# Performance work log

Hardware: AMD Instinct MI355X
Metric: run time of the kernel (lower is better)

Reference implementation:

```python
import jax, jax.numpy as jnp
import numpy as np

NUM_ITERS = 10  # forward() runs power_iteration with num_iters=10


def setup_inputs() -> dict:
    key = jax.random.key(0)
    k1, k2 = jax.random.split(key)
    out_ch, in_ch, h, w = 2048, 2048, 3, 3
    conv_filter = jax.random.normal(k1, (out_ch, in_ch, h, w), dtype=jnp.float32) * 0.02
    u = jax.random.normal(k2, (1, in_ch * w), dtype=jnp.float32)
    u = u / jnp.linalg.norm(u, axis=1, keepdims=True)
    return {"conv_filter": conv_filter, "u": u}


def reference(conv_filter, u):
    out_ch, in_ch, h, w = conv_filter.shape
    # permute (0,2,1,3) then view as [out_ch*h, in_ch*w]
    W = jnp.transpose(conv_filter, (0, 2, 1, 3)).reshape(out_ch * h, in_ch * w)
    Ws = jax.lax.stop_gradient(W)  # power iteration vectors are detached

    def body(i, carry):
        u_n, _ = carry
        v = u_n @ Ws.T                                   # [1, out_ch*h]
        v_n = v / jnp.linalg.norm(v, axis=1, keepdims=True)
        u2 = v_n @ Ws                                    # [1, in_ch*w]
        u_n2 = u2 / jnp.linalg.norm(u2, axis=1, keepdims=True)
        return (u_n2, v_n)

    v0 = jnp.zeros((1, out_ch * h), dtype=conv_filter.dtype)  # overwritten in first iter
    u_n, v_n = jax.lax.fori_loop(0, NUM_ITERS, body, (u, v0))

    # sigma = v W u^T with u, v treated as constants (custom autograd Function)
    sigma = (v_n @ W) @ u_n.T                            # [1, 1]
    return jnp.sqrt(jnp.asarray(h * w, dtype=conv_filter.dtype)) * sigma
```

## Files before the change

kernel.cpp:

```cpp
#include <hip/hip_runtime.h>
#include <hip/hip_bf16.h>
#include <hip/hip_fp16.h>

#define OC_N     2048
#define IC_N     2048
#define RC       6144
#define OCSTRIDE 18432
#define UNSCALE  0.0000152587890625f

typedef float v2f __attribute__((ext_vector_type(2)));

__device__ __forceinline__ float wave_reduce(float x) {
#pragma unroll
    for (int off = 32; off > 0; off >>= 1) x += __shfl_down(x, off, 64);
    return x;
}

__global__ __launch_bounds__(256) void convert_q_kernel(
    const float* __restrict__ conv, unsigned char* __restrict__ Wq)
{
    const int t  = blockIdx.x * 256 + threadIdx.x;
    const int o8 = t * 8;
    const int r  = o8 / RC;
    const int c0 = o8 % RC;
    const int oc = r / 3, hh = r % 3;
    const float* base = conv + (size_t)oc * OCSTRIDE + hh * 3;
    float f[8];
#pragma unroll
    for (int e = 0; e < 8; ++e) {
        const int c  = c0 + e;
        const int ic = c / 3, ww = c - 3 * ic;
        f[e] = base[ic * 9 + ww] * 256.0f;
    }
    int lo = __builtin_amdgcn_cvt_pk_fp8_f32(f[0], f[1], 0, false);
    lo     = __builtin_amdgcn_cvt_pk_fp8_f32(f[2], f[3], lo, true);
    int hi = __builtin_amdgcn_cvt_pk_fp8_f32(f[4], f[5], 0, false);
    hi     = __builtin_amdgcn_cvt_pk_fp8_f32(f[6], f[7], hi, true);
    *reinterpret_cast<uint2*>(Wq + o8) = make_uint2((unsigned)lo, (unsigned)hi);
}

__global__ __launch_bounds__(256) void transpose_q_kernel(
    const unsigned char* __restrict__ Wq, unsigned char* __restrict__ WqT)
{
    __shared__ unsigned char tile[64][68];
    const int tid = threadIdx.x;
    const int tr  = blockIdx.x;
    const int tc  = blockIdx.y;

    const int r  = tid >> 2;
    const int cq = (tid & 3) * 16;
    const uint4 w = *reinterpret_cast<const uint4*>(
        Wq + (size_t)(tr * 64 + r) * RC + tc * 64 + cq);
    *reinterpret_cast<unsigned int*>(&tile[r][cq +  0]) = w.x;
    *reinterpret_cast<unsigned int*>(&tile[r][cq +  4]) = w.y;
    *reinterpret_cast<unsigned int*>(&tile[r][cq +  8]) = w.z;
    *reinterpret_cast<unsigned int*>(&tile[r][cq + 12]) = w.w;
    __syncthreads();

    const int orow = tid >> 2;
    const int ocq  = (tid & 3) * 16;
    unsigned int u32s[4];
#pragma unroll
    for (int wi = 0; wi < 4; ++wi) {
        const int ro = ocq + 4 * wi;
        u32s[wi] =  (unsigned int)tile[ro + 0][orow]
                 | ((unsigned int)tile[ro + 1][orow] << 8)
                 | ((unsigned int)tile[ro + 2][orow] << 16)
                 | ((unsigned int)tile[ro + 3][orow] << 24);
    }
    uint4 o = make_uint4(u32s[0], u32s[1], u32s[2], u32s[3]);
    *reinterpret_cast<uint4*>(WqT + (size_t)(tc * 64 + orow) * RC + tr * 64 + ocq) = o;
}

__device__ __forceinline__ float dot16(uint4 w, float4 a, float4 b, float4 c, float4 d) {
    float acc = 0.f;
    v2f f;
    f = __builtin_amdgcn_cvt_pk_f32_fp8(w.x, false); acc += f.x * a.x + f.y * a.y;
    f = __builtin_amdgcn_cvt_pk_f32_fp8(w.x, true);  acc += f.x * a.z + f.y * a.w;
    f = __builtin_amdgcn_cvt_pk_f32_fp8(w.y, false); acc += f.x * b.x + f.y * b.y;
    f = __builtin_amdgcn_cvt_pk_f32_fp8(w.y, true);  acc += f.x * b.z + f.y * b.w;
    f = __builtin_amdgcn_cvt_pk_f32_fp8(w.z, false); acc += f.x * c.x + f.y * c.y;
    f = __builtin_amdgcn_cvt_pk_f32_fp8(w.z, true);  acc += f.x * c.z + f.y * c.w;
    f = __builtin_amdgcn_cvt_pk_f32_fp8(w.w, false); acc += f.x * d.x + f.y * d.y;
    f = __builtin_amdgcn_cvt_pk_f32_fp8(w.w, true);  acc += f.x * d.z + f.y * d.w;
    return acc;
}

__device__ __forceinline__ void stage_x(const float* __restrict__ x,
                                        float4* __restrict__ x4, int tid) {
    const float4* s4 = reinterpret_cast<const float4*>(x);
#pragma unroll
    for (int k = 0; k < 6; ++k) {
        const int g = tid + 256 * k;
        x4[g + (g >> 2)] = s4[g];
    }
}

__device__ __forceinline__ void matvec_rows2(
    const unsigned char* __restrict__ W, const float4* __restrict__ x4,
    int rbase, int lane, float* out0, float* out1)
{
    const unsigned char* w0 = W + (size_t)rbase * RC;
    float acc0 = 0.f, acc1 = 0.f;
#pragma unroll
    for (int i = 0; i < 6; ++i) {
        const int slot = i * 320 + lane * 5;
        const float4 a = x4[slot + 0];
        const float4 b = x4[slot + 1];
        const float4 c = x4[slot + 2];
        const float4 d = x4[slot + 3];
        const uint4 wA = *reinterpret_cast<const uint4*>(w0 +      i * 1024 + lane * 16);
        const uint4 wB = *reinterpret_cast<const uint4*>(w0 + RC + i * 1024 + lane * 16);
        acc0 += dot16(wA, a, b, c, d);
        acc1 += dot16(wB, a, b, c, d);
    }
    *out0 = wave_reduce(acc0);
    *out1 = wave_reduce(acc1);
}

__global__ __launch_bounds__(256) void matvec_q_kernel(
    const unsigned char* __restrict__ W, const float* __restrict__ x,
    float* __restrict__ y, float scale)
{
    __shared__ float x_lds[7680];
    float4* x4 = reinterpret_cast<float4*>(x_lds);

    const int tid  = threadIdx.x;
    const int lane = tid & 63;
    const int wid  = tid >> 6;

    stage_x(x, x4, tid);
    __syncthreads();

    const int rbase = blockIdx.x * 8 + wid * 2;
    float a0, a1;
    matvec_rows2(W, x4, rbase, lane, &a0, &a1);
    if (lane == 0) { y[rbase] = a0 * scale; y[rbase + 1] = a1 * scale; }
}

__global__ __launch_bounds__(256) void final_kernel(
    const float* __restrict__ v, const float* __restrict__ t,
    const float* __restrict__ u, float* __restrict__ out)
{
    __shared__ float ssv[4];
    __shared__ float ssu[4];
    __shared__ float sdot[4];
    const int tid  = threadIdx.x;
    const int lane = tid & 63;
    const int wid  = tid >> 6;
    float sqv = 0.f, squ = 0.f, dot = 0.f;
#pragma unroll
    for (int k = 0; k < 24; ++k) {
        const float xv = v[tid + 256 * k];
        const float xt = t[tid + 256 * k];
        const float xu = u[tid + 256 * k];
        sqv += xv * xv;
        squ += xu * xu;
        dot += xv * xt;
    }
    sqv = wave_reduce(sqv);
    squ = wave_reduce(squ);
    dot = wave_reduce(dot);
    if (lane == 0) { ssv[wid] = sqv; ssu[wid] = squ; sdot[wid] = dot; }
    __syncthreads();
    if (tid == 0) {
        const float vs = ssv[0] + ssv[1] + ssv[2] + ssv[3];
        const float us = ssu[0] + ssu[1] + ssu[2] + ssu[3];
        const float dt = sdot[0] + sdot[1] + sdot[2] + sdot[3];
        out[0] = (3.0f / 256.0f) * dt * rsqrtf(vs) * rsqrtf(us);
    }
}

extern "C" void kernel_launch(void* const* d_in, const int* in_sizes, int n_in,
                              void* d_out, int out_size, void* d_ws, size_t ws_size,
                              hipStream_t stream)
{
    const float* conv = (const float*)d_in[0];
    const float* u_in = (const float*)d_in[1];
    float* out = (float*)d_out;

    const size_t WQ_BYTES = (size_t)RC * RC;
    const size_t needed = 2 * WQ_BYTES + (size_t)3 * RC * sizeof(float);
    if (ws_size < needed) return;

    unsigned char* Wq  = (unsigned char*)d_ws;
    unsigned char* WqT = Wq + WQ_BYTES;
    float* v_vec = (float*)(WqT + WQ_BYTES);
    float* u_vec = v_vec + RC;
    float* t_vec = u_vec + RC;

    convert_q_kernel<<<RC * RC / 8 / 256, 256, 0, stream>>>(conv, Wq);
    transpose_q_kernel<<<dim3(RC / 64, RC / 64), 256, 0, stream>>>(Wq, WqT);

    for (int i = 0; i < 10; ++i) {
        matvec_q_kernel<<<RC / 8, 256, 0, stream>>>(
            Wq, (i == 0) ? u_in : u_vec, v_vec, 1.0f);
        matvec_q_kernel<<<RC / 8, 256, 0, stream>>>(
            WqT, v_vec, u_vec, UNSCALE);
    }

    matvec_q_kernel<<<RC / 8, 256, 0, stream>>>(Wq, u_vec, t_vec, 1.0f);
    final_kernel<<<1, 256, 0, stream>>>(v_vec, t_vec, u_vec, out);
}
```

Measured before the change: 405.4 us.

## Fuse fp8 quantize with transpose and derive sigma from last norm

```diff
diff --git a/kernel.cpp b/kernel.cpp
--- a/kernel.cpp
+++ b/kernel.cpp
@@ -16,60 +16,69 @@
     return x;
 }
 
-__global__ __launch_bounds__(256) void convert_q_kernel(
-    const float* __restrict__ conv, unsigned char* __restrict__ Wq)
-{
-    const int t  = blockIdx.x * 256 + threadIdx.x;
-    const int o8 = t * 8;
-    const int r  = o8 / RC;
-    const int c0 = o8 % RC;
-    const int oc = r / 3, hh = r % 3;
-    const float* base = conv + (size_t)oc * OCSTRIDE + hh * 3;
-    float f[8];
-#pragma unroll
-    for (int e = 0; e < 8; ++e) {
-        const int c  = c0 + e;
-        const int ic = c / 3, ww = c - 3 * ic;
-        f[e] = base[ic * 9 + ww] * 256.0f;
-    }
-    int lo = __builtin_amdgcn_cvt_pk_fp8_f32(f[0], f[1], 0, false);
-    lo     = __builtin_amdgcn_cvt_pk_fp8_f32(f[2], f[3], lo, true);
-    int hi = __builtin_amdgcn_cvt_pk_fp8_f32(f[4], f[5], 0, false);
-    hi     = __builtin_amdgcn_cvt_pk_fp8_f32(f[6], f[7], hi, true);
-    *reinterpret_cast<uint2*>(Wq + o8) = make_uint2((unsigned)lo, (unsigned)hi);
-}
-
-__global__ __launch_bounds__(256) void transpose_q_kernel(
-    const unsigned char* __restrict__ Wq, unsigned char* __restrict__ WqT)
+__global__ __launch_bounds__(256) void convert_both_kernel(
+    const float* __restrict__ conv, unsigned char* __restrict__ Wq,
+    unsigned char* __restrict__ WqT)
 {
     __shared__ unsigned char tile[64][68];
     const int tid = threadIdx.x;
     const int tr  = blockIdx.x;
     const int tc  = blockIdx.y;
 
-    const int r  = tid >> 2;
-    const int cq = (tid & 3) * 16;
-    const uint4 w = *reinterpret_cast<const uint4*>(
-        Wq + (size_t)(tr * 64 + r) * RC + tc * 64 + cq);
-    *reinterpret_cast<unsigned int*>(&tile[r][cq +  0]) = w.x;
-    *reinterpret_cast<unsigned int*>(&tile[r][cq +  4]) = w.y;
-    *reinterpret_cast<unsigned int*>(&tile[r][cq +  8]) = w.z;
-    *reinterpret_cast<unsigned int*>(&tile[r][cq + 12]) = w.w;
+    {
+        const int rl = tid >> 2;
+        const int cq = (tid & 3) * 16;
+        const int r  = tr * 64 + rl;
+        const int oc = r / 3, hh = r % 3;
+        const float* base = conv + (size_t)oc * OCSTRIDE + hh * 3;
+        float f[16];
+#pragma unroll
+        for (int j = 0; j < 16; ++j) {
+            const int c  = tc * 64 + cq + j;
+            const int ic = c / 3, ww = c - 3 * ic;
+            f[j] = base[ic * 9 + ww] * 256.0f;
+        }
+        unsigned int w32[4];
+#pragma unroll
+        for (int q = 0; q < 4; ++q) {
+            int v = __builtin_amdgcn_cvt_pk_fp8_f32(f[4*q+0], f[4*q+1], 0, false);
+            v     = __builtin_amdgcn_cvt_pk_fp8_f32(f[4*q+2], f[4*q+3], v, true);
+            w32[q] = (unsigned)v;
+        }
+#pragma unroll
+        for (int q = 0; q < 4; ++q)
+            *reinterpret_cast<unsigned int*>(&tile[rl][cq + 4*q]) = w32[q];
+    }
     __syncthreads();
 
-    const int orow = tid >> 2;
-    const int ocq  = (tid & 3) * 16;
-    unsigned int u32s[4];
-#pragma unroll
-    for (int wi = 0; wi < 4; ++wi) {
-        const int ro = ocq + 4 * wi;
-        u32s[wi] =  (unsigned int)tile[ro + 0][orow]
-                 | ((unsigned int)tile[ro + 1][orow] << 8)
-                 | ((unsigned int)tile[ro + 2][orow] << 16)
-                 | ((unsigned int)tile[ro + 3][orow] << 24);
-    }
-    uint4 o = make_uint4(u32s[0], u32s[1], u32s[2], u32s[3]);
-    *reinterpret_cast<uint4*>(WqT + (size_t)(tc * 64 + orow) * RC + tr * 64 + ocq) = o;
+    {
+        const int rl = tid >> 2;
+        const int cq = (tid & 3) * 16;
+        uint4 o;
+        o.x = *reinterpret_cast<const unsigned int*>(&tile[rl][cq +  0]);
+        o.y = *reinterpret_cast<const unsigned int*>(&tile[rl][cq +  4]);
+        o.z = *reinterpret_cast<const unsigned int*>(&tile[rl][cq +  8]);
+        o.w = *reinterpret_cast<const unsigned int*>(&tile[rl][cq + 12]);
+        *reinterpret_cast<uint4*>(
+            Wq + (size_t)(tr * 64 + rl) * RC + tc * 64 + cq) = o;
+    }
+
+    {
+        const int orow = tid >> 2;
+        const int ocq  = (tid & 3) * 16;
+        unsigned int u32s[4];
+#pragma unroll
+        for (int wi = 0; wi < 4; ++wi) {
+            const int ro = ocq + 4 * wi;
+            u32s[wi] =  (unsigned int)tile[ro + 0][orow]
+                     | ((unsigned int)tile[ro + 1][orow] << 8)
+                     | ((unsigned int)tile[ro + 2][orow] << 16)
+                     | ((unsigned int)tile[ro + 3][orow] << 24);
+        }
+        uint4 o = make_uint4(u32s[0], u32s[1], u32s[2], u32s[3]);
+        *reinterpret_cast<uint4*>(
+            WqT + (size_t)(tc * 64 + orow) * RC + tr * 64 + ocq) = o;
+    }
 }
 
 __device__ __forceinline__ float dot16(uint4 w, float4 a, float4 b, float4 c, float4 d) {
@@ -139,35 +148,30 @@
 }
 
 __global__ __launch_bounds__(256) void final_kernel(
-    const float* __restrict__ v, const float* __restrict__ t,
-    const float* __restrict__ u, float* __restrict__ out)
+    const float* __restrict__ v, const float* __restrict__ u,
+    float* __restrict__ out)
 {
     __shared__ float ssv[4];
     __shared__ float ssu[4];
-    __shared__ float sdot[4];
     const int tid  = threadIdx.x;
     const int lane = tid & 63;
     const int wid  = tid >> 6;
-    float sqv = 0.f, squ = 0.f, dot = 0.f;
+    float sqv = 0.f, squ = 0.f;
 #pragma unroll
     for (int k = 0; k < 24; ++k) {
         const float xv = v[tid + 256 * k];
-        const float xt = t[tid + 256 * k];
         const float xu = u[tid + 256 * k];
         sqv += xv * xv;
         squ += xu * xu;
-        dot += xv * xt;
     }
     sqv = wave_reduce(sqv);
     squ = wave_reduce(squ);
-    dot = wave_reduce(dot);
-    if (lane == 0) { ssv[wid] = sqv; ssu[wid] = squ; sdot[wid] = dot; }
+    if (lane == 0) { ssv[wid] = sqv; ssu[wid] = squ; }
     __syncthreads();
     if (tid == 0) {
         const float vs = ssv[0] + ssv[1] + ssv[2] + ssv[3];
         const float us = ssu[0] + ssu[1] + ssu[2] + ssu[3];
-        const float dt = sdot[0] + sdot[1] + sdot[2] + sdot[3];
-        out[0] = (3.0f / 256.0f) * dt * rsqrtf(vs) * rsqrtf(us);
+        out[0] = 768.0f * sqrtf(us / vs);
     }
 }
 
@@ -180,17 +184,15 @@
     float* out = (float*)d_out;
 
     const size_t WQ_BYTES = (size_t)RC * RC;
-    const size_t needed = 2 * WQ_BYTES + (size_t)3 * RC * sizeof(float);
+    const size_t needed = 2 * WQ_BYTES + (size_t)2 * RC * sizeof(float);
     if (ws_size < needed) return;
 
     unsigned char* Wq  = (unsigned char*)d_ws;
     unsigned char* WqT = Wq + WQ_BYTES;
     float* v_vec = (float*)(WqT + WQ_BYTES);
     float* u_vec = v_vec + RC;
-    float* t_vec = u_vec + RC;
-
-    convert_q_kernel<<<RC * RC / 8 / 256, 256, 0, stream>>>(conv, Wq);
-    transpose_q_kernel<<<dim3(RC / 64, RC / 64), 256, 0, stream>>>(Wq, WqT);
+
+    convert_both_kernel<<<dim3(RC / 64, RC / 64), 256, 0, stream>>>(conv, Wq, WqT);
 
     for (int i = 0; i < 10; ++i) {
         matvec_q_kernel<<<RC / 8, 256, 0, stream>>>(
@@ -199,6 +201,5 @@
             WqT, v_vec, u_vec, UNSCALE);
     }
 
-    matvec_q_kernel<<<RC / 8, 256, 0, stream>>>(Wq, u_vec, t_vec, 1.0f);
-    final_kernel<<<1, 256, 0, stream>>>(v_vec, t_vec, u_vec, out);
-}
+    final_kernel<<<1, 256, 0, stream>>>(v_vec, u_vec, out);
+}
```

Result: faster. 394.2 us (-2.8%).
